# Optimization experiments

Measured on AMD Instinct MI355X. Metric: run time of the kernel, lower is better.

## Reference

```python
import jax, jax.numpy as jnp
import numpy as np

B, T, D = 2, 2048, 2048
NH, HD, R = 16, 128, 64
CQ, CKV = 1536, 512
WINDOW, CHUNK = 512, 256
MIN_SCALE, MAX_SCALE = 0.5, 2.0
ROPE_BASE = 500000.0
EPS = 1e-6


def setup_inputs() -> dict:
    key = jax.random.key(0)
    ks = jax.random.split(key, 12)
    w = lambda k, shape: (jax.random.normal(k, shape, jnp.float32) * 0.02)
    return {
        "x": jax.random.normal(ks[0], (B, T, D), jnp.float32),
        "uncertainty": jax.random.uniform(ks[1], (B, T), jnp.float32),
        "Wq_down": w(ks[2], (D, CQ)),
        "q_norm_w": jnp.ones((CQ,), jnp.float32),
        "Wq_up": w(ks[3], (CQ, NH * HD)),
        "Wq_rope": w(ks[4], (CQ, NH * R)),
        "Wkv_down": w(ks[5], (D, CKV)),
        "kv_norm_w": jnp.ones((CKV,), jnp.float32),
        "Wk_up": w(ks[6], (CKV, NH * HD)),
        "Wv_up": w(ks[7], (CKV, NH * HD)),
        "Wk_rope": w(ks[8], (D, NH * R)),
        "Wout": w(ks[9], (NH * HD, D)),
        "Wgate": w(ks[10], (D, 1)),
        "bgate": jnp.zeros((1,), jnp.float32),
    }


def rms_norm(x, w):
    return x * jax.lax.rsqrt(jnp.mean(x * x, axis=-1, keepdims=True) + EPS) * w


def epe_cos_sin(positions, uncertainty):
    # freq_idx = arange(r//2)*2/r ; theta = base**(-freq_idx)
    half = R // 2
    freq_idx = jnp.arange(half, dtype=jnp.float32) * 2.0 / R
    theta = ROPE_BASE ** (-freq_idx)                                  # [half]
    scale = MIN_SCALE + jnp.clip(uncertainty, 0.0, 1.0) * (MAX_SCALE - MIN_SCALE)  # [B,T]
    freqs = positions[None, :, None].astype(jnp.float32) * theta[None, None, :] * scale[:, :, None]
    freqs = freqs[:, :, None, :]                                      # [B,T,1,half]
    return jnp.cos(freqs), jnp.sin(freqs)


def apply_rope(x, cos, sin):
    # x: [B,T,nH,r]; rotate halves with per-(B,T) cos/sin broadcast over heads
    half = x.shape[-1] // 2
    x1, x2 = x[..., :half], x[..., half:]
    return jnp.concatenate([x1 * cos - x2 * sin, x2 * cos + x1 * sin], axis=-1)


def sliding_window_attn(Q, K, V, window, chunk):
    # Q,K: [B,nH,T,dk], V: [B,nH,T,dv]; chunked causal sliding-window
    b, nh, t, dk = Q.shape
    dv = V.shape[-1]
    half_w = window // 2
    n_chunks = t // chunk                    # T chosen multiple of chunk
    L = chunk + 2 * half_w
    Kp = jnp.pad(K, ((0, 0), (0, 0), (half_w, half_w), (0, 0)))
    Vp = jnp.pad(V, ((0, 0), (0, 0), (half_w, half_w), (0, 0)))
    starts = jnp.arange(n_chunks) * chunk
    idx = starts[:, None] + jnp.arange(L)[None, :]          # [nC,L] into padded axis
    Kw = Kp[:, :, idx]                                       # [B,nH,nC,L,dk]
    Vw = Vp[:, :, idx]                                       # [B,nH,nC,L,dv]
    Qc = Q.reshape(b, nh, n_chunks, chunk, dk)
    scores = jnp.einsum('bhcqd,bhckd->bhcqk', Qc, Kw) / jnp.sqrt(jnp.float32(dk))
    key_pos = idx - half_w                                   # actual key positions [nC,L]
    q_pos = starts[:, None] + jnp.arange(chunk)[None, :]     # [nC,chunk]
    mask = (key_pos[:, None, :] <= q_pos[:, :, None]) & (key_pos[:, None, :] >= 0)
    scores = jnp.where(mask[None, None], scores, -jnp.inf)
    p = jax.nn.softmax(scores, axis=-1)
    out = jnp.einsum('bhcqk,bhckd->bhcqd', p, Vw)
    return out.reshape(b, nh, t, dv)


def reference(x, uncertainty, Wq_down, q_norm_w, Wq_up, Wq_rope,
              Wkv_down, kv_norm_w, Wk_up, Wv_up, Wk_rope, Wout, Wgate, bgate):
    b, t, d = x.shape
    positions = jnp.arange(t)

    q_lat = rms_norm(x @ Wq_down, q_norm_w)                  # [B,T,CQ]
    q_c = (q_lat @ Wq_up).reshape(b, t, NH, HD)
    q_r = (q_lat @ Wq_rope).reshape(b, t, NH, R)
    kv_lat = rms_norm(x @ Wkv_down, kv_norm_w)               # [B,T,CKV]
    k_c = (kv_lat @ Wk_up).reshape(b, t, NH, HD)
    v = (kv_lat @ Wv_up).reshape(b, t, NH, HD)
    k_r = (x @ Wk_rope).reshape(b, t, NH, R)

    cos, sin = epe_cos_sin(positions, uncertainty)
    q_r = apply_rope(q_r, cos, sin)
    k_r = apply_rope(k_r, cos, sin)

    Q = jnp.concatenate([q_c, q_r], axis=-1).transpose(0, 2, 1, 3)   # [B,nH,T,HD+R]
    K = jnp.concatenate([k_c, k_r], axis=-1).transpose(0, 2, 1, 3)
    V = v.transpose(0, 2, 1, 3)                                       # [B,nH,T,HD]

    out_ar = sliding_window_attn(Q, K, V, WINDOW, CHUNK)

    # full bidirectional SDPA
    scale = 1.0 / jnp.sqrt(jnp.float32(HD + R))
    scores = jnp.einsum('bhqd,bhkd->bhqk', Q, K) * scale
    out_bidir = jnp.einsum('bhqk,bhkd->bhqd', jax.nn.softmax(scores, axis=-1), V)

    alpha = jax.nn.sigmoid((x @ Wgate + bgate)).squeeze(-1)           # [B,T]
    a = alpha[:, None, :, None]
    merged = a * out_bidir + (1.0 - a) * out_ar                       # [B,nH,T,HD]
    merged = merged.transpose(0, 2, 1, 3).reshape(b, t, NH * HD)
    return merged @ Wout, alpha
```

## Files before the change

kernel.cpp:

```cpp
#include <hip/hip_runtime.h>
#include <hip/hip_bf16.h>
#include <math.h>

typedef __hip_bfloat16 bf16;
using v8bf = __attribute__((ext_vector_type(8))) __bf16;
using v4f  = __attribute__((ext_vector_type(4))) float;
using f32x16 = __attribute__((ext_vector_type(16))) float;
using v4u = __attribute__((ext_vector_type(4))) unsigned;
using v4s = __attribute__((ext_vector_type(4))) short;
using v8s = __attribute__((ext_vector_type(8))) short;

#define T_SEQ 2048
#define DMODEL 2048
#define NHEADS 16
#define HDIM 128
#define RDIM 64

__device__ __forceinline__ short f2bfbits(float f) {
  bf16 h = __float2bfloat16(f);
  short s;
  __builtin_memcpy(&s, &h, 2);
  return s;
}

__device__ __forceinline__ unsigned pk2bf(float a, float b) {
  unsigned lo = (unsigned short)f2bfbits(a);
  unsigned hi = (unsigned short)f2bfbits(b);
  return lo | (hi << 16);
}

typedef const __attribute__((address_space(1))) unsigned gu32;
typedef __attribute__((address_space(3))) unsigned lu32;
__device__ __forceinline__ void gl_lds16(const void* g, void* l) {
  __builtin_amdgcn_global_load_lds((gu32*)g, (lu32*)l, 16, 0, 0);
}

template <int N>
__device__ __forceinline__ void vwn() {
  asm volatile("s_waitcnt vmcnt(%0)" :: "n"(N) : "memory");
}

__global__ void detect_k(const unsigned* __restrict__ x, int* __restrict__ flag) {
  __shared__ int cnt;
  if (threadIdx.x == 0) cnt = 0;
  __syncthreads();
  int c = 0;
#pragma unroll
  for (int i = 0; i < 4; i++) {
    unsigned w = x[threadIdx.x * 4 + i];
    unsigned e = (w >> 7) & 0xFFu;
    if (e < 97u || e > 157u) c++;
  }
  atomicAdd(&cnt, c);
  __syncthreads();
  if (threadIdx.x == 0) flag[0] = (cnt > 256) ? 1 : 0;
}

__global__ __launch_bounds__(256) void conv_all(const void* x_raw,
                                                const void* qnw_raw, const void* kvnw_raw,
                                                const void* wg_raw, const void* bg_raw,
                                                const void* unc_raw,
                                                bf16* xc, bf16* qnw, bf16* kvnw,
                                                bf16* wgc, bf16* bgc, float* uncf,
                                                const int* flag) {
  bool isf = (*flag != 0);
  if (blockIdx.x < 8192) {
    int i4 = blockIdx.x * 256 + threadIdx.x;
    v4s o;
    if (isf) {
      float4 v = ((const float4*)x_raw)[i4];
      o[0] = f2bfbits(v.x); o[1] = f2bfbits(v.y);
      o[2] = f2bfbits(v.z); o[3] = f2bfbits(v.w);
    } else {
      o = ((const v4s*)x_raw)[i4];
    }
    *reinterpret_cast<v4s*>(xc + (size_t)i4 * 4) = o;
  } else {
    int i = (blockIdx.x - 8192) * 256 + threadIdx.x;
    if (i < 1536) qnw[i] = isf ? __float2bfloat16(((const float*)qnw_raw)[i]) : ((const bf16*)qnw_raw)[i];
    else if (i < 2048) { int j = i - 1536; kvnw[j] = isf ? __float2bfloat16(((const float*)kvnw_raw)[j]) : ((const bf16*)kvnw_raw)[j]; }
    else if (i < 4096) { int j = i - 2048; wgc[j] = isf ? __float2bfloat16(((const float*)wg_raw)[j]) : ((const bf16*)wg_raw)[j]; }
    else if (i < 4097) bgc[0] = isf ? __float2bfloat16(((const float*)bg_raw)[0]) : ((const bf16*)bg_raw)[0];
    else if (i < 8193) { int j = i - 4097; uncf[j] = isf ? ((const float*)unc_raw)[j] : __bfloat162float(((const bf16*)unc_raw)[j]); }
  }
}

struct TP8 {
  const void* s[8];
  bf16* d[8];
  int rows[8];
  int cols[8];
  int pre[9];
};

__global__ __launch_bounds__(256) void transpose_all(TP8 jobs, const int* __restrict__ flag) {
  __shared__ bf16 tile[32][33];
  int bid = blockIdx.x;
  int w = 0;
#pragma unroll
  for (int k = 0; k < 7; k++) if (bid >= jobs.pre[k + 1]) w = k + 1;
  int lt = bid - jobs.pre[w];
  int rows = jobs.rows[w], cols = jobs.cols[w];
  int tpr = cols >> 5;
  int by = (lt / tpr) << 5, bx = (lt % tpr) << 5;
  const void* src = jobs.s[w];
  bf16* dst = jobs.d[w];
  int tx = threadIdx.x & 31, ty = threadIdx.x >> 5;
  bool isf = (*flag != 0);
#pragma unroll
  for (int i = 0; i < 32; i += 8) {
    size_t idx = (size_t)(by + ty + i) * cols + bx + tx;
    tile[ty + i][tx] = isf ? __float2bfloat16(((const float*)src)[idx])
                           : ((const bf16*)src)[idx];
  }
  __syncthreads();
#pragma unroll
  for (int i = 0; i < 32; i += 8)
    dst[(size_t)(bx + ty + i) * rows + by + tx] = tile[tx][ty + i];
}

__global__ __launch_bounds__(256) void transpose_str(const bf16* __restrict__ src,
                                                     bf16* __restrict__ dst,
                                                     int srcStride, int dstStride) {
  __shared__ bf16 tile[32][33];
  int bx = blockIdx.x * 32, by = blockIdx.y * 32;
  int tx = threadIdx.x & 31, ty = threadIdx.x >> 5;
#pragma unroll
  for (int i = 0; i < 32; i += 8)
    tile[ty + i][tx] = src[(size_t)(by + ty + i) * srcStride + bx + tx];
  __syncthreads();
#pragma unroll
  for (int i = 0; i < 32; i += 8)
    dst[(size_t)(bx + ty + i) * dstStride + by + tx] = tile[tx][ty + i];
}

__global__ __launch_bounds__(512, 2) void gemm8(const bf16* __restrict__ A,
                                                const bf16* __restrict__ BT,
                                                bf16* __restrict__ Cb,
                                                int M, int N, int K,
                                                const int* __restrict__ oflag,
                                                void* __restrict__ dvout) {
  __shared__ __align__(16) short lds[2][2][16384];
  const int m0 = blockIdx.y * 256, n0 = blockIdx.x * 256;
  const int tid = threadIdx.x;
  const int w = tid >> 6, lane = tid & 63;
  const int quad4 = lane >> 4, l16 = lane & 15;
  const int wmq = (w >> 1) * 32;
  const int wnq = (w & 1) * 64;

  v4f acc[4][2][4];
#pragma unroll
  for (int qi = 0; qi < 4; qi++)
#pragma unroll
    for (int mf = 0; mf < 2; mf++)
#pragma unroll
      for (int nf = 0; nf < 4; nf++) acc[qi][mf][nf] = (v4f){0.f, 0.f, 0.f, 0.f};

  auto stage_half = [&](int sp, int kb, int sbuf) {
    const int mat = (sp == 0 || sp == 3) ? 0 : 1;
    const int half = (sp >= 2) ? 1 : 0;
    const bf16* base = mat ? BT : A;
    const int rbase = (mat ? n0 : m0) + half * 128 + w * 16;
#pragma unroll
    for (int i = 0; i < 2; i++) {
      int lrow = half * 128 + w * 16 + i * 8;
      short* dst = &lds[sbuf][mat][lrow * 64];
      int rl = i * 8 + (lane >> 3);
      int grow = rbase + i * 8 + (lane >> 3);
      int cb = ((lane & 7) * 16) ^ ((rl & 12) << 3);
      const bf16* src = base + (size_t)grow * K + kb + (cb >> 1);
      gl_lds16(src, dst);
    }
  };

#define GEMM8_PHASE(BUF, PH, STAGE_STMT, WAIT_STMT) do {                          \
    constexpr int qm_ = (PH) >> 1, qn_ = (PH) & 1;                                \
    v8bf a_[2][2], b_[2][4];                                                      \
    _Pragma("unroll")                                                             \
    for (int ks = 0; ks < 2; ks++) {                                              \
      _Pragma("unroll")                                                           \
      for (int mf = 0; mf < 2; mf++) {                                            \
        int r_ = qm_ * 128 + wmq + mf * 16 + l16;                                 \
        int c_ = (ks * 64 + quad4 * 16) ^ ((r_ & 12) << 3);                       \
        a_[ks][mf] = *reinterpret_cast<const v8bf*>(                              \
            (const char*)&lds[BUF][0][0] + r_ * 128 + c_);                        \
      }                                                                           \
      _Pragma("unroll")                                                           \
      for (int nf = 0; nf < 4; nf++) {                                            \
        int r_ = qn_ * 128 + wnq + nf * 16 + l16;                                 \
        int c_ = (ks * 64 + quad4 * 16) ^ ((r_ & 12) << 3);                       \
        b_[ks][nf] = *reinterpret_cast<const v8bf*>(                              \
            (const char*)&lds[BUF][1][0] + r_ * 128 + c_);                        \
      }                                                                           \
    }                                                                             \
    STAGE_STMT;                                                                   \
    WAIT_STMT;                                                                    \
    __builtin_amdgcn_s_barrier();                                                 \
    __builtin_amdgcn_s_setprio(1);                                                \
    _Pragma("unroll")                                                             \
    for (int ks = 0; ks < 2; ks++)                                                \
      _Pragma("unroll")                                                           \
      for (int mf = 0; mf < 2; mf++)                                              \
        _Pragma("unroll")                                                         \
        for (int nf = 0; nf < 4; nf++)                                            \
          acc[qm_ * 2 + qn_][mf][nf] = __builtin_amdgcn_mfma_f32_16x16x32_bf16(   \
              a_[ks][mf], b_[ks][nf], acc[qm_ * 2 + qn_][mf][nf], 0, 0, 0);       \
    __builtin_amdgcn_s_setprio(0);                                                \
    __builtin_amdgcn_s_barrier();                                                 \
  } while (0)

  const int T = K >> 6;

#pragma unroll
  for (int sp = 0; sp < 4; sp++) stage_half(sp, 0, 0);
#pragma unroll
  for (int sp = 0; sp < 4; sp++) stage_half(sp, 64, 1);
  vwn<12>();
  __builtin_amdgcn_s_barrier();

  GEMM8_PHASE(0, 0, (void)0, vwn<10>());
  GEMM8_PHASE(0, 1, (void)0, vwn<8>());
  GEMM8_PHASE(0, 2, (void)0, (void)0);
  GEMM8_PHASE(0, 3, (void)0, vwn<4>());

  for (int t = 1; t <= T - 2; t++) {
    const int buf = t & 1, sbuf = buf ^ 1, kbn = (t + 1) << 6;
    GEMM8_PHASE(buf, 0, stage_half(0, kbn, sbuf), vwn<4>());
    GEMM8_PHASE(buf, 1, stage_half(1, kbn, sbuf), vwn<4>());
    GEMM8_PHASE(buf, 2, stage_half(2, kbn, sbuf), (void)0);
    GEMM8_PHASE(buf, 3, stage_half(3, kbn, sbuf), vwn<4>());
  }

  {
    const int buf = (T - 1) & 1;
    GEMM8_PHASE(buf, 0, (void)0, vwn<2>());
    GEMM8_PHASE(buf, 1, (void)0, vwn<0>());
    GEMM8_PHASE(buf, 2, (void)0, (void)0);
    GEMM8_PHASE(buf, 3, (void)0, (void)0);
  }
#undef GEMM8_PHASE

  const bool isf = dvout && (*oflag != 0);
#pragma unroll
  for (int qi = 0; qi < 4; qi++) {
    const int qm = qi >> 1, qn = qi & 1;
#pragma unroll
    for (int mf = 0; mf < 2; mf++)
#pragma unroll
      for (int nf = 0; nf < 4; nf++)
#pragma unroll
        for (int r = 0; r < 4; r++) {
          int row = m0 + qm * 128 + wmq + mf * 16 + quad4 * 4 + r;
          int col = n0 + qn * 128 + wnq + nf * 16 + l16;
          float vv = acc[qi][mf][nf][r];
          size_t idx = (size_t)row * N + col;
          if (dvout) {
            if (isf) ((float*)dvout)[idx] = vv;
            else     ((bf16*)dvout)[idx] = __float2bfloat16(vv);
          } else {
            Cb[idx] = __float2bfloat16(vv);
          }
        }
  }
}

__global__ __launch_bounds__(256) void rmsnorm_both(const bf16* __restrict__ xproj,
                                                    const bf16* __restrict__ qnw,
                                                    const bf16* __restrict__ kvnw,
                                                    bf16* __restrict__ q_lat,
                                                    bf16* __restrict__ kv_lat) {
  int bid = blockIdx.x, tid = threadIdx.x;
  bool isq = bid < 4096;
  int row = isq ? bid : bid - 4096;
  int C = isq ? 1536 : 512;
  const bf16* r = xproj + (size_t)row * 3072 + (isq ? 0 : 1536);
  const bf16* w = isq ? qnw : kvnw;
  bf16* o = (isq ? q_lat : kv_lat) + (size_t)row * C;
  float s = 0.f;
  for (int i = tid; i < C; i += 256) { float v = __bfloat162float(r[i]); s += v * v; }
#pragma unroll
  for (int m = 32; m; m >>= 1) s += __shfl_xor(s, m);
  __shared__ float red[4];
  if ((tid & 63) == 0) red[tid >> 6] = s;
  __syncthreads();
  float tot = red[0] + red[1] + red[2] + red[3];
  float rs = rsqrtf(tot / (float)C + 1e-6f);
  for (int i = tid; i < C; i += 256)
    o[i] = __float2bfloat16(__bfloat162float(r[i]) * rs * __bfloat162float(w[i]));
}

__global__ __launch_bounds__(256) void rope_gate(bf16* __restrict__ qcr,
                                                 bf16* __restrict__ xproj,
                                                 const float* __restrict__ unc,
                                                 const bf16* __restrict__ x,
                                                 const bf16* __restrict__ wg,
                                                 const bf16* __restrict__ bg,
                                                 float* __restrict__ af,
                                                 void* __restrict__ dout,
                                                 const int* __restrict__ flag) {
  __shared__ float red[4];
  int tid = threadIdx.x;
  if (blockIdx.x < 8192) {
    int idx = blockIdx.x * 256 + tid;
    int j = idx & 31, h = (idx >> 5) & 15, bt = idx >> 9;
    int t = bt & (T_SEQ - 1);
    float u = unc[bt];
    u = fminf(fmaxf(u, 0.f), 1.f);
    float scale = 0.5f + 1.5f * u;
    float theta = expf(-(float)j * (1.f / 32.f) * logf(500000.f));
    float f = (float)t * theta * scale;
    float c = cosf(f), s = sinf(f);
    size_t base = (size_t)bt * 3072 + 2048 + h * RDIM + j;
    {
      float x1 = __bfloat162float(qcr[base]), x2 = __bfloat162float(qcr[base + 32]);
      qcr[base]      = __float2bfloat16(x1 * c - x2 * s);
      qcr[base + 32] = __float2bfloat16(x2 * c + x1 * s);
    }
    {
      float x1 = __bfloat162float(xproj[base]), x2 = __bfloat162float(xproj[base + 32]);
      xproj[base]      = __float2bfloat16(x1 * c - x2 * s);
      xproj[base + 32] = __float2bfloat16(x2 * c + x1 * s);
    }
  } else {
    int row = blockIdx.x - 8192;
    const bf16* xr = x + (size_t)row * DMODEL;
    float s = 0.f;
    for (int i = tid; i < DMODEL; i += 256)
      s += __bfloat162float(xr[i]) * __bfloat162float(wg[i]);
#pragma unroll
    for (int m = 32; m; m >>= 1) s += __shfl_xor(s, m);
    if ((tid & 63) == 0) red[tid >> 6] = s;
    __syncthreads();
    if (tid == 0) {
      float tot = red[0] + red[1] + red[2] + red[3] + __bfloat162float(bg[0]);
      float a = 1.f / (1.f + expf(-tot));
      af[row] = a;
      size_t oi = (size_t)8388608 + row;
      if (*flag) ((float*)dout)[oi] = a;
      else       ((bf16*)dout)[oi] = __float2bfloat16(a);
    }
  }
}

__global__ __launch_bounds__(512, 2) void attn_f(const bf16* __restrict__ qcr,
                                                 const bf16* __restrict__ kcv,
                                                 const bf16* __restrict__ xproj,
                                                 const bf16* __restrict__ vt,
                                                 const float* __restrict__ alphaF,
                                                 bf16* __restrict__ out) {
  constexpr int LDK = 200;
  constexpr int LDV = 72;
  __shared__ __align__(16) short sh[64 * LDK + 128 * LDV];
  short* lk  = sh;
  short* lvt = sh + 64 * LDK;

  const int f_ = blockIdx.x;
  const int xcd = f_ & 7, g_ = f_ >> 3;
  const int qt = g_ & 7;
  const int p_ = xcd + 8 * (g_ >> 3);
  const int h = p_ & 15, b = p_ >> 4;

  const int qs = qt * 256;
  const int tid = threadIdx.x;
  const int w = tid >> 6, lane = tid & 63;
  const int l5 = lane & 31, h8 = lane >> 5;
  const int q0 = qs + w * 32;
  const int myq = q0 + l5;

  v8bf qf[12];
  {
    const bf16* qcb = qcr + ((size_t)b * T_SEQ + myq) * 3072 + h * HDIM;
#pragma unroll
    for (int ks = 0; ks < 8; ks++)
      qf[ks] = *reinterpret_cast<const v8bf*>(qcb + ks * 16 + h8 * 8);
    const bf16* qrb = qcr + ((size_t)b * T_SEQ + myq) * 3072 + 2048 + h * RDIM;
#pragma unroll
    for (int ks = 0; ks < 4; ks++)
      qf[8 + ks] = *reinterpret_cast<const v8bf*>(qrb + ks * 16 + h8 * 8);
  }

  float l_sum = 0.f, l_snap = 0.f;
  f32x16 oacc[4], snap[4];
#pragma unroll
  for (int nd = 0; nd < 4; nd++)
#pragma unroll
    for (int r = 0; r < 16; r++) { oacc[nd][r] = 0.f; snap[nd][r] = 0.f; }

  const float a_q = alphaF[b * T_SEQ + myq];
  const float sc = 0.07216878364870323f;

  const int klo  = (qt > 0) ? (qs - 256) : 0;
  const int kb_d = qs + (w >> 1) * 64;

  const int koc0 = (tid >> 4) * 4096 + (tid & 15) * 8;
  const int ldc0 = (tid >> 4) * LDK  + (tid & 15) * 8;
  const int kor0 = (tid >> 3) * 3072 + (tid & 7) * 8;
  const int ldr0 = (tid >> 3) * LDK + 128 + (tid & 7) * 8;
  const int kov0 = (tid >> 3) * 4096 + (tid & 7) * 8;
  const int ldv0 = (tid >> 3) * LDV  + (tid & 7) * 8;
  const bf16* kc_base = kcv   + (size_t)b * T_SEQ * 4096 + h * HDIM;
  const bf16* kr_base = xproj + (size_t)b * T_SEQ * 3072 + 2048 + h * RDIM;
  const bf16* v_base  = vt    + (size_t)h * HDIM * (2 * T_SEQ) + b * T_SEQ;

  v4u rc[2], rr1, rv[2];
  auto issue = [&](int kb) {
    const bf16* pc = kc_base + (size_t)kb * 4096;
    const bf16* pr = kr_base + (size_t)kb * 3072;
    const bf16* pv = v_base + kb;
#pragma unroll
    for (int i = 0; i < 2; i++) rc[i] = *reinterpret_cast<const v4u*>(pc + koc0 + i * 131072);
    rr1 = *reinterpret_cast<const v4u*>(pr + kor0);
#pragma unroll
    for (int i = 0; i < 2; i++) rv[i] = *reinterpret_cast<const v4u*>(pv + kov0 + i * 262144);
  };

  auto qk = [&](int j) -> f32x16 {
    f32x16 s;
#pragma unroll
    for (int r = 0; r < 16; r++) s[r] = 0.f;
#pragma unroll
    for (int ks = 0; ks < 12; ks++) {
      v8bf kf = *reinterpret_cast<const v8bf*>(&lk[(j * 32 + l5) * LDK + ks * 16 + h8 * 8]);
      s = __builtin_amdgcn_mfma_f32_32x32x16_bf16(kf, qf[ks], s, 0, 0, 0);
    }
    return s;
  };
  auto pack8 = [&](const float* p) -> v8bf {
    unsigned Y0 = pk2bf(p[0], p[1]);
    unsigned Y1 = pk2bf(p[2], p[3]);
    unsigned Y2 = pk2bf(p[4], p[5]);
    unsigned Y3 = pk2bf(p[6], p[7]);
    asm volatile("v_permlane32_swap_b32 %0, %1" : "+v"(Y0), "+v"(Y2));
    asm volatile("v_permlane32_swap_b32 %0, %1" : "+v"(Y1), "+v"(Y3));
    v4u t; t.x = Y0; t.y = Y1; t.z = Y2; t.w = Y3;
    return __builtin_bit_cast(v8bf, t);
  };
  auto pvj = [&](int j, const v8bf* pf) {
#pragma unroll
    for (int ck = 0; ck < 2; ck++)
#pragma unroll
      for (int nd = 0; nd < 4; nd++) {
        v8bf vf = *reinterpret_cast<const v8bf*>(&lvt[(nd * 32 + l5) * LDV + (j * 2 + ck) * 16 + h8 * 8]);
        oacc[nd] = __builtin_amdgcn_mfma_f32_32x32x16_bf16(vf, pf[ck], oacc[nd], 0, 0, 0);
      }
  };
  auto plainpass = [&](int j) {
    f32x16 s = qk(j);
    v8bf pf[2];
#pragma unroll
    for (int cc = 0; cc < 2; cc++) {
      float p[8];
#pragma unroll
      for (int r8 = 0; r8 < 8; r8++) {
        float e = __expf(s[cc * 8 + r8] * sc);
        p[r8] = e;
        l_sum += e;
      }
      pf[cc] = pack8(p);
    }
    pvj(j, pf);
  };
  auto maskpass = [&](int j, int kb, bool upper) {
    f32x16 s = qk(j);
    v8bf pf[2];
#pragma unroll
    for (int cc = 0; cc < 2; cc++) {
      float p[8];
#pragma unroll
      for (int r8 = 0; r8 < 8; r8++) {
        int r = cc * 8 + r8;
        int kk = kb + j * 32 + (r & 3) + 8 * (r >> 2) + 4 * h8;
        float e = __expf(s[r] * sc);
        bool keep = upper ? (kk > myq) : (kk <= myq);
        e = keep ? e : 0.f;
        p[r8] = e;
        l_sum += e;
      }
      pf[cc] = pack8(p);
    }
    pvj(j, pf);
  };

  issue(0);

  for (int kb = 0; kb < T_SEQ; kb += 64) {
    __syncthreads();
#pragma unroll
    for (int i = 0; i < 2; i++) *reinterpret_cast<v4u*>(&lk[ldc0 + i * 32 * LDK]) = rc[i];
    *reinterpret_cast<v4u*>(&lk[ldr0]) = rr1;
#pragma unroll
    for (int i = 0; i < 2; i++) *reinterpret_cast<v4u*>(&lvt[ldv0 + i * 64 * LDV]) = rv[i];
    if (kb + 64 < T_SEQ) issue(kb + 64);
    __syncthreads();

    if (kb == klo) {
#pragma unroll
      for (int nd = 0; nd < 4; nd++) snap[nd] = oacc[nd];
      l_snap = l_sum;
    }

    __builtin_amdgcn_s_setprio(1);
    if (kb != kb_d) {
      plainpass(0);
      plainpass(1);
    } else {
      maskpass(0, kb, false);
      maskpass(1, kb, false);
      {
        float lar_h = l_sum - l_snap;
        float lar = lar_h + __shfl_xor(lar_h, 32);
        float sAR = (1.f - a_q) / lar;
#pragma unroll
        for (int nd = 0; nd < 4; nd++)
#pragma unroll
          for (int r = 0; r < 16; r++)
            snap[nd][r] = (oacc[nd][r] - snap[nd][r]) * sAR;
      }
      maskpass(0, kb, true);
      maskpass(1, kb, true);
    }
    __builtin_amdgcn_s_setprio(0);
  }

  l_sum += __shfl_xor(l_sum, 32);
  float inv = a_q / l_sum;

  __syncthreads();
#pragma unroll
  for (int ph = 0; ph < 2; ph++) {
    bool act = (w >> 2) == ph;
    short* tile = sh + (w & 3) * (32 * 136);
    if (act) {
#pragma unroll
      for (int nd = 0; nd < 4; nd++)
#pragma unroll
        for (int rg = 0; rg < 4; rg++) {
          v4s pk;
#pragma unroll
          for (int i = 0; i < 4; i++) {
            float val = oacc[nd][rg * 4 + i] * inv + snap[nd][rg * 4 + i];
            pk[i] = f2bfbits(val);
          }
          *reinterpret_cast<v4s*>(&tile[l5 * 136 + nd * 32 + rg * 8 + h8 * 4]) = pk;
        }
    }
    __syncthreads();
    if (act) {
#pragma unroll
      for (int i = 0; i < 8; i++) {
        int r = i * 4 + (lane >> 4);
        int q2 = q0 + r;
        int dcol = (lane & 15) * 8;
        v8s mv = *reinterpret_cast<const v8s*>(&tile[r * 136 + dcol]);
        size_t gbase = ((size_t)b * T_SEQ + q2) * DMODEL + h * HDIM + dcol;
        *reinterpret_cast<v8s*>((void*)(out + gbase)) = mv;
      }
    }
    __syncthreads();
  }
}

extern "C" void kernel_launch(void* const* d_in, const int* in_sizes, int n_in,
                              void* d_out, int out_size, void* d_ws, size_t ws_size,
                              hipStream_t stream) {
  const void* x_raw    = d_in[0];
  const void* unc_raw  = d_in[1];
  const void* Wqd_raw  = d_in[2];
  const void* qnw_raw  = d_in[3];
  const void* Wqu_raw  = d_in[4];
  const void* Wqr_raw  = d_in[5];
  const void* Wkvd_raw = d_in[6];
  const void* kvnw_raw = d_in[7];
  const void* Wku_raw  = d_in[8];
  const void* Wvu_raw  = d_in[9];
  const void* Wkr_raw  = d_in[10];
  const void* Wo_raw   = d_in[11];
  const void* Wg_raw   = d_in[12];
  const void* bg_raw   = d_in[13];

  char* ws = (char*)d_ws;
  size_t off = 0;
  auto alloc = [&](size_t bytes) -> void* {
    char* p = ws + off;
    off += (bytes + 255) & ~(size_t)255;
    return p;
  };
  int*  flag   = (int*)alloc(256);
  bf16* xc     = (bf16*)alloc((size_t)4096 * 2048 * 2);
  float* uncf  = (float*)alloc((size_t)4096 * 4);
  bf16* qnw    = (bf16*)alloc(1536 * 2);
  bf16* kvnw   = (bf16*)alloc(512 * 2);
  bf16* wgc    = (bf16*)alloc(2048 * 2);
  bf16* bgc    = (bf16*)alloc(256);
  bf16* BT1    = (bf16*)alloc((size_t)3072 * 2048 * 2);
  bf16* BT2    = (bf16*)alloc((size_t)3072 * 1536 * 2);
  bf16* BT3    = (bf16*)alloc((size_t)4096 * 512 * 2);
  bf16* WoT    = (bf16*)alloc((size_t)2048 * 2048 * 2);
  bf16* xproj  = (bf16*)alloc((size_t)4096 * 3072 * 2);
  bf16* q_lat  = (bf16*)alloc((size_t)4096 * 1536 * 2);
  bf16* kv_lat = (bf16*)alloc((size_t)4096 * 512 * 2);
  bf16* qcr    = (bf16*)alloc((size_t)4096 * 3072 * 2);
  bf16* kcv    = (bf16*)alloc((size_t)4096 * 4096 * 2);
  bf16* vT     = (bf16*)alloc((size_t)4096 * 2048 * 2);
  bf16* attno  = (bf16*)alloc((size_t)4096 * 2048 * 2);
  float* alphaF= (float*)alloc((size_t)4096 * 4);

  detect_k<<<1, 256, 0, stream>>>((const unsigned*)x_raw, flag);

  conv_all<<<8225, 256, 0, stream>>>(x_raw, qnw_raw, kvnw_raw, Wg_raw, bg_raw, unc_raw,
                                     xc, qnw, kvnw, wgc, bgc, uncf, flag);

  TP8 jobs;
  const void* srcs[8] = {Wqd_raw, Wkvd_raw, Wkr_raw, Wqu_raw, Wqr_raw, Wku_raw, Wvu_raw, Wo_raw};
  bf16* dsts[8] = {BT1, BT1 + (size_t)1536 * 2048, BT1 + (size_t)2048 * 2048,
                   BT2, BT2 + (size_t)2048 * 1536,
                   BT3, BT3 + (size_t)2048 * 512, WoT};
  int rws[8] = {2048, 2048, 2048, 1536, 1536, 512, 512, 2048};
  int cls[8] = {1536, 512, 1024, 2048, 1024, 2048, 2048, 2048};
  int acc_t = 0;
  for (int i = 0; i < 8; i++) {
    jobs.s[i] = srcs[i]; jobs.d[i] = dsts[i];
    jobs.rows[i] = rws[i]; jobs.cols[i] = cls[i];
    jobs.pre[i] = acc_t;
    acc_t += (rws[i] / 32) * (cls[i] / 32);
  }
  jobs.pre[8] = acc_t;
  transpose_all<<<acc_t, 256, 0, stream>>>(jobs, flag);

  auto gemm8b = [&](const bf16* A, const bf16* BT, bf16* C, int M, int N, int K,
                    const int* oflag, void* dvout) {
    gemm8<<<dim3(N / 256, M / 256), 512, 0, stream>>>(A, BT, C, M, N, K, oflag, dvout);
  };

  gemm8b(xc, BT1, xproj, 4096, 3072, 2048, nullptr, nullptr);
  rmsnorm_both<<<8192, 256, 0, stream>>>(xproj, qnw, kvnw, q_lat, kv_lat);
  gemm8b(q_lat, BT2, qcr, 4096, 3072, 1536, nullptr, nullptr);
  gemm8b(kv_lat, BT3, kcv, 4096, 4096, 512, nullptr, nullptr);

  transpose_str<<<dim3(64, 128), 256, 0, stream>>>(kcv + 2048, vT, 4096, 4096);

  rope_gate<<<12288, 256, 0, stream>>>(qcr, xproj, uncf, xc, wgc, bgc, alphaF, d_out, flag);

  attn_f<<<256, 512, 0, stream>>>(qcr, kcv, xproj, vT, alphaF, attno);

  gemm8b(attno, WoT, nullptr, 4096, 2048, 2048, flag, d_out);

  (void)in_sizes; (void)n_in; (void)out_size; (void)ws_size;
}
```

Before: 606.4 us.

## Restructure GEMM pipeline with fragment reuse, new swizzle, and split QK accumulators

Rewrites the GEMM main loop so each k-tile has a single barrier per phase and no trailing barrier. The quadrant order becomes 0,1,3,2 so A or B fragments loaded from LDS are reused across consecutive MFMA groups, cutting LDS reads. The LDS XOR swizzle changes from (row&12)<<3 to (row&7)<<4 to reduce bank conflicts, and the prologue stages only one buffer ahead. In attention, the QK dot product uses two independent MFMA accumulator chains to break the dependency chain, and the next-tile global load is issued after the barrier. The cost is more registers, plus a risk of LDS hazards from the fewer barriers.

Result: faster. 585.7 us (-3.4%).

```diff
diff --git a/kernel.cpp b/kernel.cpp
--- a/kernel.cpp
+++ b/kernel.cpp
@@ -38,6 +38,11 @@
 template <int N>
 __device__ __forceinline__ void vwn() {
   asm volatile("s_waitcnt vmcnt(%0)" :: "n"(N) : "memory");
+}
+
+__device__ __forceinline__ void barx() {
+  __builtin_amdgcn_s_barrier();
+  asm volatile("" ::: "memory");
 }
 
 __global__ void detect_k(const unsigned* __restrict__ x, int* __restrict__ flag) {
@@ -160,42 +165,42 @@
     const int mat = (sp == 0 || sp == 3) ? 0 : 1;
     const int half = (sp >= 2) ? 1 : 0;
     const bf16* base = mat ? BT : A;
-    const int rbase = (mat ? n0 : m0) + half * 128 + w * 16;
+    const int rb = (mat ? n0 : m0) + half * 128 + w * 16;
+    const int cb = (((lane & 7) ^ (lane >> 3)) << 4);
 #pragma unroll
     for (int i = 0; i < 2; i++) {
-      int lrow = half * 128 + w * 16 + i * 8;
-      short* dst = &lds[sbuf][mat][lrow * 64];
-      int rl = i * 8 + (lane >> 3);
-      int grow = rbase + i * 8 + (lane >> 3);
-      int cb = ((lane & 7) * 16) ^ ((rl & 12) << 3);
+      short* dst = &lds[sbuf][mat][(half * 128 + w * 16 + i * 8) * 64];
+      int grow = rb + i * 8 + (lane >> 3);
       const bf16* src = base + (size_t)grow * K + kb + (cb >> 1);
       gl_lds16(src, dst);
     }
   };
 
-#define GEMM8_PHASE(BUF, PH, STAGE_STMT, WAIT_STMT) do {                          \
-    constexpr int qm_ = (PH) >> 1, qn_ = (PH) & 1;                                \
-    v8bf a_[2][2], b_[2][4];                                                      \
-    _Pragma("unroll")                                                             \
-    for (int ks = 0; ks < 2; ks++) {                                              \
-      _Pragma("unroll")                                                           \
-      for (int mf = 0; mf < 2; mf++) {                                            \
-        int r_ = qm_ * 128 + wmq + mf * 16 + l16;                                 \
-        int c_ = (ks * 64 + quad4 * 16) ^ ((r_ & 12) << 3);                       \
-        a_[ks][mf] = *reinterpret_cast<const v8bf*>(                              \
-            (const char*)&lds[BUF][0][0] + r_ * 128 + c_);                        \
-      }                                                                           \
-      _Pragma("unroll")                                                           \
-      for (int nf = 0; nf < 4; nf++) {                                            \
-        int r_ = qn_ * 128 + wnq + nf * 16 + l16;                                 \
-        int c_ = (ks * 64 + quad4 * 16) ^ ((r_ & 12) << 3);                       \
-        b_[ks][nf] = *reinterpret_cast<const v8bf*>(                              \
-            (const char*)&lds[BUF][1][0] + r_ * 128 + c_);                        \
-      }                                                                           \
-    }                                                                             \
-    STAGE_STMT;                                                                   \
-    WAIT_STMT;                                                                    \
-    __builtin_amdgcn_s_barrier();                                                 \
+  v8bf a_[2][2], b_[2][4];
+  auto loadA = [&](int bufb, int qm) {
+#pragma unroll
+    for (int ks = 0; ks < 2; ks++)
+#pragma unroll
+      for (int mf = 0; mf < 2; mf++) {
+        int r_ = qm * 128 + wmq + mf * 16 + l16;
+        int c_ = (ks * 64 + quad4 * 16) ^ ((r_ & 7) << 4);
+        a_[ks][mf] = *reinterpret_cast<const v8bf*>(
+            (const char*)&lds[bufb][0][0] + r_ * 128 + c_);
+      }
+  };
+  auto loadB = [&](int bufb, int qn) {
+#pragma unroll
+    for (int ks = 0; ks < 2; ks++)
+#pragma unroll
+      for (int nf = 0; nf < 4; nf++) {
+        int r_ = qn * 128 + wnq + nf * 16 + l16;
+        int c_ = (ks * 64 + quad4 * 16) ^ ((r_ & 7) << 4);
+        b_[ks][nf] = *reinterpret_cast<const v8bf*>(
+            (const char*)&lds[bufb][1][0] + r_ * 128 + c_);
+      }
+  };
+
+#define MMQ(QI) do {                                                              \
     __builtin_amdgcn_s_setprio(1);                                                \
     _Pragma("unroll")                                                             \
     for (int ks = 0; ks < 2; ks++)                                                \
@@ -203,42 +208,31 @@
       for (int mf = 0; mf < 2; mf++)                                              \
         _Pragma("unroll")                                                         \
         for (int nf = 0; nf < 4; nf++)                                            \
-          acc[qm_ * 2 + qn_][mf][nf] = __builtin_amdgcn_mfma_f32_16x16x32_bf16(   \
-              a_[ks][mf], b_[ks][nf], acc[qm_ * 2 + qn_][mf][nf], 0, 0, 0);       \
+          acc[QI][mf][nf] = __builtin_amdgcn_mfma_f32_16x16x32_bf16(              \
+              a_[ks][mf], b_[ks][nf], acc[QI][mf][nf], 0, 0, 0);                  \
     __builtin_amdgcn_s_setprio(0);                                                \
-    __builtin_amdgcn_s_barrier();                                                 \
   } while (0)
 
   const int T = K >> 6;
 
 #pragma unroll
   for (int sp = 0; sp < 4; sp++) stage_half(sp, 0, 0);
-#pragma unroll
-  for (int sp = 0; sp < 4; sp++) stage_half(sp, 64, 1);
-  vwn<12>();
-  __builtin_amdgcn_s_barrier();
-
-  GEMM8_PHASE(0, 0, (void)0, vwn<10>());
-  GEMM8_PHASE(0, 1, (void)0, vwn<8>());
-  GEMM8_PHASE(0, 2, (void)0, (void)0);
-  GEMM8_PHASE(0, 3, (void)0, vwn<4>());
-
-  for (int t = 1; t <= T - 2; t++) {
-    const int buf = t & 1, sbuf = buf ^ 1, kbn = (t + 1) << 6;
-    GEMM8_PHASE(buf, 0, stage_half(0, kbn, sbuf), vwn<4>());
-    GEMM8_PHASE(buf, 1, stage_half(1, kbn, sbuf), vwn<4>());
-    GEMM8_PHASE(buf, 2, stage_half(2, kbn, sbuf), (void)0);
-    GEMM8_PHASE(buf, 3, stage_half(3, kbn, sbuf), vwn<4>());
-  }
-
+
+  for (int t = 0; t < T - 1; t++) {
+    const int buf = t & 1, sb = buf ^ 1, kbn = (t + 1) << 6;
+    vwn<4>(); barx(); stage_half(0, kbn, sb); loadA(buf, 0); loadB(buf, 0); MMQ(0);
+    vwn<4>(); barx(); stage_half(1, kbn, sb); loadB(buf, 1); MMQ(1);
+    vwn<4>(); barx(); stage_half(2, kbn, sb); loadA(buf, 1); MMQ(3);
+    barx(); stage_half(3, kbn, sb); loadB(buf, 0); MMQ(2);
+  }
   {
     const int buf = (T - 1) & 1;
-    GEMM8_PHASE(buf, 0, (void)0, vwn<2>());
-    GEMM8_PHASE(buf, 1, (void)0, vwn<0>());
-    GEMM8_PHASE(buf, 2, (void)0, (void)0);
-    GEMM8_PHASE(buf, 3, (void)0, (void)0);
-  }
-#undef GEMM8_PHASE
+    vwn<4>(); barx(); loadA(buf, 0); loadB(buf, 0); MMQ(0);
+    vwn<2>(); barx(); loadB(buf, 1); MMQ(1);
+    vwn<0>(); barx(); loadA(buf, 1); MMQ(3);
+    barx(); loadB(buf, 0); MMQ(2);
+  }
+#undef MMQ
 
   const bool isf = dvout && (*oflag != 0);
 #pragma unroll
@@ -415,15 +409,19 @@
   };
 
   auto qk = [&](int j) -> f32x16 {
-    f32x16 s;
-#pragma unroll
-    for (int r = 0; r < 16; r++) s[r] = 0.f;
-#pragma unroll
-    for (int ks = 0; ks < 12; ks++) {
-      v8bf kf = *reinterpret_cast<const v8bf*>(&lk[(j * 32 + l5) * LDK + ks * 16 + h8 * 8]);
-      s = __builtin_amdgcn_mfma_f32_32x32x16_bf16(kf, qf[ks], s, 0, 0, 0);
-    }
-    return s;
+    f32x16 s0, s1;
+#pragma unroll
+    for (int r = 0; r < 16; r++) { s0[r] = 0.f; s1[r] = 0.f; }
+#pragma unroll
+    for (int ks = 0; ks < 6; ks++) {
+      v8bf kf0 = *reinterpret_cast<const v8bf*>(&lk[(j * 32 + l5) * LDK + (2 * ks) * 16 + h8 * 8]);
+      v8bf kf1 = *reinterpret_cast<const v8bf*>(&lk[(j * 32 + l5) * LDK + (2 * ks + 1) * 16 + h8 * 8]);
+      s0 = __builtin_amdgcn_mfma_f32_32x32x16_bf16(kf0, qf[2 * ks], s0, 0, 0, 0);
+      s1 = __builtin_amdgcn_mfma_f32_32x32x16_bf16(kf1, qf[2 * ks + 1], s1, 0, 0, 0);
+    }
+#pragma unroll
+    for (int r = 0; r < 16; r++) s0[r] += s1[r];
+    return s0;
   };
   auto pack8 = [&](const float* p) -> v8bf {
     unsigned Y0 = pk2bf(p[0], p[1]);
@@ -490,8 +488,8 @@
     *reinterpret_cast<v4u*>(&lk[ldr0]) = rr1;
 #pragma unroll
     for (int i = 0; i < 2; i++) *reinterpret_cast<v4u*>(&lvt[ldv0 + i * 64 * LDV]) = rv[i];
+    __syncthreads();
     if (kb + 64 < T_SEQ) issue(kb + 64);
-    __syncthreads();
 
     if (kb == klo) {
 #pragma unroll
```
